# Optimization experiments

Measured on AMD Instinct MI355X. Metric: run time of the kernel, lower is better.

Reference implementation:

```python
import jax, jax.numpy as jnp
import numpy as np

N, E, D = 20000, 320000, 256
EPS = 1e-5


def setup_inputs() -> dict:
    key = jax.random.key(0)
    ks = jax.random.split(key, 12)
    s = 1.0 / np.sqrt(D)
    s2 = 1.0 / np.sqrt(2 * D)
    return {
        "node_embeddings": jax.random.normal(ks[0], (N, D), jnp.float32),
        "edge_index": jax.random.randint(ks[1], (2, E), 0, N, jnp.int64),
        "edge_embeddings": jax.random.normal(ks[2], (E, D), jnp.float32),
        # message MLP: Linear(D,D) -> GELU -> Linear(D,D)
        "W1m": jax.random.uniform(ks[3], (D, D), jnp.float32, -s, s),
        "b1m": jnp.zeros((D,), jnp.float32),
        "W2m": jax.random.uniform(ks[4], (D, D), jnp.float32, -s, s),
        "b2m": jnp.zeros((D,), jnp.float32),
        # update MLP: Linear(D,2D) -> GELU -> Linear(2D,D)
        "W1u": jax.random.uniform(ks[5], (D, 2 * D), jnp.float32, -s, s),
        "b1u": jnp.zeros((2 * D,), jnp.float32),
        "W2u": jax.random.uniform(ks[6], (2 * D, D), jnp.float32, -s2, s2),
        "b2u": jnp.zeros((D,), jnp.float32),
        # LayerNorm params
        "gamma": jnp.ones((D,), jnp.float32),
        "beta": jnp.zeros((D,), jnp.float32),
    }


def _layer_norm(x, gamma, beta):
    mu = jnp.mean(x, axis=-1, keepdims=True)
    var = jnp.mean(jnp.square(x - mu), axis=-1, keepdims=True)
    return (x - mu) * jax.lax.rsqrt(var + EPS) * gamma + beta


def reference(node_embeddings, edge_index, edge_embeddings,
              W1m, b1m, W2m, b2m, W1u, b1u, W2u, b2u, gamma, beta):
    src = edge_index[0]
    dst = edge_index[1]
    n = node_embeddings.shape[0]
    # gather + edge add + message MLP (exact erf GELU, as torch default)
    h = node_embeddings[src] + edge_embeddings           # [E, D]
    h = jax.nn.gelu(h @ W1m + b1m, approximate=False)
    messages = h @ W2m + b2m                             # [E, D]
    # scatter-mean aggregation
    agg = jax.ops.segment_sum(messages, dst, num_segments=n)  # [N, D]
    deg = jax.ops.segment_sum(jnp.ones((dst.shape[0], 1), node_embeddings.dtype),
                              dst, num_segments=n)            # [N, 1]
    agg = agg / jnp.maximum(deg, 1.0)
    # update MLP + residual + LayerNorm
    u = jax.nn.gelu(agg @ W1u + b1u, approximate=False) @ W2u + b2u
    return _layer_norm(node_embeddings + u, gamma, beta)
```

## Files before the change

kernel.cpp:

```cpp
#include <hip/hip_runtime.h>
#include <hip/hip_bf16.h>

#define N_NODES 20000
#define N_EDGES 320000

typedef __attribute__((ext_vector_type(8))) short short8;
typedef __attribute__((ext_vector_type(4))) float f32x4;

static __device__ __forceinline__ unsigned short f2bf(float f) {
  __hip_bfloat16 h = __float2bfloat16(f);
  union { __hip_bfloat16 h; unsigned short u; } cv; cv.h = h; return cv.u;
}

static __device__ __forceinline__ float bf2f(unsigned short u) {
  union { unsigned int u; float f; } cv; cv.u = ((unsigned int)u) << 16; return cv.f;
}

static __device__ __forceinline__ unsigned int pk2(float a, float b) {
  return (unsigned int)f2bf(a) | ((unsigned int)f2bf(b) << 16);
}

static __device__ __forceinline__ float gelu_f(float x) {
  float z = x * (2.3022082f + 0.1029432f * x * x);
  z = fminf(fmaxf(z, -30.0f), 30.0f);
  float t = exp2f(z);
  return x * t * __frcp_rn(1.0f + t);
}

#define SWZ(row, byteoff) ((byteoff) ^ (((row) & 7) << 4))
#define SWZU(b) ((b) ^ ((((b) >> 8) & 7) << 4))

__global__ void zero_kernel(float4* __restrict__ S4, int4* __restrict__ cnt4) {
  int idx = blockIdx.x * blockDim.x + threadIdx.x;
  S4[idx] = make_float4(0.f, 0.f, 0.f, 0.f);
  if (idx < N_NODES / 4) cnt4[idx] = make_int4(0, 0, 0, 0);
}

__global__ void pack_kernel(const float* __restrict__ W1m, const float* __restrict__ W2m,
                            const float* __restrict__ W1u, const float* __restrict__ W2u,
                            unsigned short* __restrict__ P1m, unsigned short* __restrict__ P2m,
                            unsigned short* __restrict__ P1u, unsigned short* __restrict__ P2u) {
  int idx = blockIdx.x * blockDim.x + threadIdx.x;
  const float* W; unsigned short* P; int K, Nc, local;
  if (idx < 65536)        { W = W1m; P = P1m; K = 256; Nc = 256; local = idx; }
  else if (idx < 131072)  { W = W2m; P = P2m; K = 256; Nc = 256; local = idx - 65536; }
  else if (idx < 262144)  { W = W1u; P = P1u; K = 256; Nc = 512; local = idx - 131072; }
  else                    { W = W2u; P = P2u; K = 512; Nc = 256; local = idx - 262144; }
  int frag = local >> 9, wi = local & 511;
  int l = wi >> 3, i = wi & 7;
  int kf = K >> 5;
  int cf = frag / kf, t = frag % kf;
  int k = t * 32 + (l >> 4) * 8 + i;
  int n = cf * 16 + (l & 15);
  P[local] = f2bf(W[(size_t)k * Nc + n]);
}

__global__ void hist_kernel(const int* __restrict__ dst, int* __restrict__ cnt) {
  int e = blockIdx.x * blockDim.x + threadIdx.x;
  atomicAdd(&cnt[dst[e]], 1);
}

__global__ __launch_bounds__(1024) void scan_kernel(const int* __restrict__ cnt,
                                                    int* __restrict__ rptr,
                                                    int* __restrict__ cur) {
  __shared__ int sums[1024];
  const int t = threadIdx.x;
  const int base = t * 20;
  int local[20];
  int s = 0;
#pragma unroll
  for (int i = 0; i < 20; ++i) {
    int idx = base + i;
    int v = (idx < N_NODES) ? cnt[idx] : 0;
    local[i] = s;
    s += v;
  }
  int v = s;
  sums[t] = v;
  for (int off = 1; off < 1024; off <<= 1) {
    __syncthreads();
    int o = (t >= off) ? sums[t - off] : 0;
    __syncthreads();
    v += o;
    sums[t] = v;
  }
  int excl = v - s;
#pragma unroll
  for (int i = 0; i < 20; ++i) {
    int idx = base + i;
    if (idx < N_NODES) { int p = excl + local[i]; rptr[idx] = p; cur[idx] = p; }
  }
  if (t == 1023) rptr[N_NODES] = v;
}

__global__ void scatter_kernel(const int* __restrict__ dst, int* __restrict__ cur,
                               int* __restrict__ perm) {
  int e = blockIdx.x * blockDim.x + threadIdx.x;
  int d = dst[e];
  int pos = atomicAdd(&cur[d], 1);
  perm[pos] = e;
}

__global__ __launch_bounds__(256) void edge_kernel(
    const float* __restrict__ node, const float* __restrict__ eemb,
    const int* __restrict__ src, const int* __restrict__ dst,
    const int* __restrict__ perm,
    const unsigned short* __restrict__ P1m, const float* __restrict__ b1m,
    float* __restrict__ S) {
  __shared__ unsigned short tA[64 * 256];
  __shared__ int dstS[64];
  const int tid = threadIdx.x;
  const int e0 = blockIdx.x * 64;
  {
    const int r = tid >> 2;
    const int cs = (tid & 3) * 64;
    const int e = perm[e0 + r];
    const int se = src[e];
    if ((tid & 3) == 0) dstS[r] = dst[e];
    const float* ep = eemb + (size_t)e * 256 + cs;
    const float* np = node + (size_t)se * 256 + cs;
#pragma unroll
    for (int i = 0; i < 8; ++i) {
      float4 a = *(const float4*)(ep + i * 8);
      float4 b = *(const float4*)(np + i * 8);
      float4 c = *(const float4*)(ep + i * 8 + 4);
      float4 d = *(const float4*)(np + i * 8 + 4);
      uint4 p;
      p.x = pk2(a.x + b.x, a.y + b.y);
      p.y = pk2(a.z + b.z, a.w + b.w);
      p.z = pk2(c.x + d.x, c.y + d.y);
      p.w = pk2(c.z + d.z, c.w + d.w);
      *(uint4*)((char*)tA + SWZ(r, r * 512 + (cs + i * 8) * 2)) = p;
    }
  }
  __syncthreads();

  const int w = tid >> 6, l = tid & 63;
  const int lr = l & 15, lh = l >> 4;
  f32x4 acc[4][4];
#pragma unroll
  for (int c = 0; c < 4; ++c) {
    float bb = b1m[w * 64 + c * 16 + lr];
#pragma unroll
    for (int r4 = 0; r4 < 4; ++r4) acc[r4][c] = f32x4{bb, bb, bb, bb};
  }
#pragma unroll
  for (int t = 0; t < 8; ++t) {
    short8 af[4], bfr[4];
#pragma unroll
    for (int r4 = 0; r4 < 4; ++r4) {
      int row = r4 * 16 + lr;
      af[r4] = *(const short8*)((const char*)tA + SWZ(row, row * 512 + t * 64 + lh * 16));
    }
#pragma unroll
    for (int c = 0; c < 4; ++c)
      bfr[c] = *(const short8*)(P1m + (size_t)(((w * 4 + c) * 8 + t) * 512 + l * 8));
#pragma unroll
    for (int r4 = 0; r4 < 4; ++r4)
#pragma unroll
      for (int c = 0; c < 4; ++c)
        acc[r4][c] = __builtin_amdgcn_mfma_f32_16x16x32_bf16(af[r4], bfr[c], acc[r4][c], 0, 0, 0);
  }
  __syncthreads();

#pragma unroll
  for (int r4 = 0; r4 < 4; ++r4)
#pragma unroll
    for (int c = 0; c < 4; ++c) {
      int col = w * 64 + c * 16 + lr;
#pragma unroll
      for (int j = 0; j < 4; ++j) {
        int row = r4 * 16 + lh * 4 + j;
        *(unsigned short*)((char*)tA + SWZ(row, row * 512 + col * 2)) =
            f2bf(gelu_f(acc[r4][c][j]));
      }
    }
  __syncthreads();

  {
    const int col = tid;
    const int r0 = 0, r1 = 32;
    float runA = 0.f, runB = 0.f;
    int curA = dstS[r0], curB = dstS[r1];
#pragma unroll 8
    for (int i = 0; i < 32; ++i) {
      int dA = dstS[r0 + i];
      int dB = dstS[r1 + i];
      float vA = bf2f(*(const unsigned short*)((const char*)tA +
                      SWZ(r0 + i, (r0 + i) * 512 + col * 2)));
      float vB = bf2f(*(const unsigned short*)((const char*)tA +
                      SWZ(r1 + i, (r1 + i) * 512 + col * 2)));
      if (dA != curA) { atomicAdd(&S[(size_t)curA * 256 + col], runA); runA = 0.f; curA = dA; }
      if (dB != curB) { atomicAdd(&S[(size_t)curB * 256 + col], runB); runB = 0.f; curB = dB; }
      runA += vA;
      runB += vB;
    }
    atomicAdd(&S[(size_t)curA * 256 + col], runA);
    atomicAdd(&S[(size_t)curB * 256 + col], runB);
  }
}

__global__ __launch_bounds__(256) void node_kernel(
    const float* __restrict__ node, const float* __restrict__ S, const int* __restrict__ rptr,
    const unsigned short* __restrict__ P2m, const float* __restrict__ b2m,
    const unsigned short* __restrict__ P1u, const float* __restrict__ b1u,
    const unsigned short* __restrict__ P2u, const float* __restrict__ b2u,
    const float* __restrict__ gamma, const float* __restrict__ beta,
    float* __restrict__ out) {
  __shared__ unsigned short tAB[2][64 * 256];
  __shared__ unsigned short tH[64 * 512];
  __shared__ float fmu[64], frs[64], fflag[64];
  float* tU = (float*)tAB;
  const int tid = threadIdx.x;
  const int n0 = blockIdx.x * 64;
  const int r = tid >> 2;
  const int cs = (tid & 3) * 64;
  const int n = n0 + r;
  const bool valid = n < N_NODES;
  {
    int dgi = valid ? (rptr[n + 1] - rptr[n]) : 0;
    float dg = (float)dgi;
    float rec = 1.0f / fmaxf(dg, 1.0f);
    if ((tid & 3) == 0) fflag[r] = (dgi > 0) ? 1.0f : 0.0f;
    const float4* sp = (const float4*)(S + (size_t)n * 256 + cs);
#pragma unroll
    for (int i = 0; i < 8; ++i) {
      float4 a = valid ? sp[2 * i]     : make_float4(0.f, 0.f, 0.f, 0.f);
      float4 b = valid ? sp[2 * i + 1] : make_float4(0.f, 0.f, 0.f, 0.f);
      uint4 p;
      p.x = pk2(a.x * rec, a.y * rec);
      p.y = pk2(a.z * rec, a.w * rec);
      p.z = pk2(b.x * rec, b.y * rec);
      p.w = pk2(b.z * rec, b.w * rec);
      *(uint4*)((char*)tAB[0] + SWZ(r, r * 512 + (cs + i * 8) * 2)) = p;
    }
  }
  __syncthreads();
  const int w = tid >> 6, l = tid & 63, lr = l & 15, lh = l >> 4;

  {
    f32x4 acc[4][4];
#pragma unroll
    for (int r4 = 0; r4 < 4; ++r4)
#pragma unroll
      for (int c = 0; c < 4; ++c) acc[r4][c] = f32x4{0.f, 0.f, 0.f, 0.f};
#pragma unroll
    for (int t = 0; t < 8; ++t) {
      short8 af[4], bfr[4];
#pragma unroll
      for (int r4 = 0; r4 < 4; ++r4) {
        int row = r4 * 16 + lr;
        af[r4] = *(const short8*)((const char*)tAB[0] + SWZ(row, row * 512 + t * 64 + lh * 16));
      }
#pragma unroll
      for (int c = 0; c < 4; ++c)
        bfr[c] = *(const short8*)(P2m + (size_t)(((w * 4 + c) * 8 + t) * 512 + l * 8));
#pragma unroll
      for (int r4 = 0; r4 < 4; ++r4)
#pragma unroll
        for (int c = 0; c < 4; ++c)
          acc[r4][c] = __builtin_amdgcn_mfma_f32_16x16x32_bf16(af[r4], bfr[c], acc[r4][c], 0, 0, 0);
    }
#pragma unroll
    for (int r4 = 0; r4 < 4; ++r4)
#pragma unroll
      for (int c = 0; c < 4; ++c) {
        int col = w * 64 + c * 16 + lr;
        float bm = b2m[col];
#pragma unroll
        for (int j = 0; j < 4; ++j) {
          int row = r4 * 16 + lh * 4 + j;
          float v = acc[r4][c][j] + fflag[row] * bm;
          *(unsigned short*)((char*)tAB[1] + SWZ(row, row * 512 + col * 2)) = f2bf(v);
        }
      }
  }
  __syncthreads();

  {
    f32x4 acc[4][8];
#pragma unroll
    for (int r4 = 0; r4 < 4; ++r4)
#pragma unroll
      for (int c = 0; c < 8; ++c) acc[r4][c] = f32x4{0.f, 0.f, 0.f, 0.f};
#pragma unroll
    for (int t = 0; t < 8; ++t) {
      short8 af[4], bfr[8];
#pragma unroll
      for (int r4 = 0; r4 < 4; ++r4) {
        int row = r4 * 16 + lr;
        af[r4] = *(const short8*)((const char*)tAB[1] + SWZ(row, row * 512 + t * 64 + lh * 16));
      }
#pragma unroll
      for (int c = 0; c < 8; ++c)
        bfr[c] = *(const short8*)(P1u + (size_t)(((w * 8 + c) * 8 + t) * 512 + l * 8));
#pragma unroll
      for (int r4 = 0; r4 < 4; ++r4)
#pragma unroll
        for (int c = 0; c < 8; ++c)
          acc[r4][c] = __builtin_amdgcn_mfma_f32_16x16x32_bf16(af[r4], bfr[c], acc[r4][c], 0, 0, 0);
    }
#pragma unroll
    for (int r4 = 0; r4 < 4; ++r4)
#pragma unroll
      for (int c = 0; c < 8; ++c) {
        int col = w * 128 + c * 16 + lr;
        float b1 = b1u[col];
#pragma unroll
        for (int j = 0; j < 4; ++j) {
          int row = r4 * 16 + lh * 4 + j;
          float v = gelu_f(acc[r4][c][j] + b1);
          *(unsigned short*)((char*)tH + SWZ(row, row * 1024 + col * 2)) = f2bf(v);
        }
      }
  }
  __syncthreads();

  {
    f32x4 acc[4][4];
#pragma unroll
    for (int r4 = 0; r4 < 4; ++r4)
#pragma unroll
      for (int c = 0; c < 4; ++c) acc[r4][c] = f32x4{0.f, 0.f, 0.f, 0.f};
#pragma unroll
    for (int t = 0; t < 16; ++t) {
      short8 af[4], bfr[4];
#pragma unroll
      for (int r4 = 0; r4 < 4; ++r4) {
        int row = r4 * 16 + lr;
        af[r4] = *(const short8*)((const char*)tH + SWZ(row, row * 1024 + t * 64 + lh * 16));
      }
#pragma unroll
      for (int c = 0; c < 4; ++c)
        bfr[c] = *(const short8*)(P2u + (size_t)(((w * 4 + c) * 16 + t) * 512 + l * 8));
#pragma unroll
      for (int r4 = 0; r4 < 4; ++r4)
#pragma unroll
        for (int c = 0; c < 4; ++c)
          acc[r4][c] = __builtin_amdgcn_mfma_f32_16x16x32_bf16(af[r4], bfr[c], acc[r4][c], 0, 0, 0);
    }
#pragma unroll
    for (int r4 = 0; r4 < 4; ++r4)
#pragma unroll
      for (int c = 0; c < 4; ++c) {
        int col = w * 64 + c * 16 + lr;
        float b2 = b2u[col];
#pragma unroll
        for (int j = 0; j < 4; ++j) {
          int row = r4 * 16 + lh * 4 + j;
          *(float*)((char*)tU + SWZU(row * 1024 + col * 4)) = acc[r4][c][j] + b2;
        }
      }
  }
  __syncthreads();

  {
    float sum = 0.f, sq = 0.f;
#pragma unroll
    for (int i = 0; i < 16; ++i) {
      int byte = SWZU(r * 1024 + (cs + i * 4) * 4);
      float4 v = *(float4*)((char*)tU + byte);
      if (valid) {
        const float4 nb = *(const float4*)(node + (size_t)n * 256 + cs + i * 4);
        v.x += nb.x; v.y += nb.y; v.z += nb.z; v.w += nb.w;
        *(float4*)((char*)tU + byte) = v;
      }
      sum += v.x + v.y + v.z + v.w;
      sq += v.x * v.x + v.y * v.y + v.z * v.z + v.w * v.w;
    }
    sum += __shfl_xor(sum, 1); sum += __shfl_xor(sum, 2);
    sq  += __shfl_xor(sq, 1);  sq  += __shfl_xor(sq, 2);
    if ((tid & 3) == 0) {
      float mu = sum * (1.0f / 256.0f);
      fmu[r] = mu;
      frs[r] = rsqrtf(fmaxf(sq * (1.0f / 256.0f) - mu * mu, 0.0f) + 1e-5f);
    }
  }
  __syncthreads();
#pragma unroll
  for (int i = 0; i < 16; ++i) {
    int f4 = i * 256 + tid;
    int row = f4 >> 6;
    int c4 = f4 & 63;
    int nn = n0 + row;
    if (nn < N_NODES) {
      float4 v = *(float4*)((char*)tU + SWZU(row * 1024 + c4 * 16));
      float mu = fmu[row], rs = frs[row];
      float4 g  = *(const float4*)(gamma + c4 * 4);
      float4 bt = *(const float4*)(beta + c4 * 4);
      float4 o;
      o.x = (v.x - mu) * rs * g.x + bt.x;
      o.y = (v.y - mu) * rs * g.y + bt.y;
      o.z = (v.z - mu) * rs * g.z + bt.z;
      o.w = (v.w - mu) * rs * g.w + bt.w;
      *(float4*)(out + (size_t)nn * 256 + c4 * 4) = o;
    }
  }
}

extern "C" void kernel_launch(void* const* d_in, const int* in_sizes, int n_in,
                              void* d_out, int out_size, void* d_ws, size_t ws_size,
                              hipStream_t stream) {
  const float* node = (const float*)d_in[0];
  const int* eidx = (const int*)d_in[1];
  const float* eemb = (const float*)d_in[2];
  const float* W1m = (const float*)d_in[3];
  const float* b1m = (const float*)d_in[4];
  const float* W2m = (const float*)d_in[5];
  const float* b2m = (const float*)d_in[6];
  const float* W1u = (const float*)d_in[7];
  const float* b1u = (const float*)d_in[8];
  const float* W2u = (const float*)d_in[9];
  const float* b2u = (const float*)d_in[10];
  const float* gamma = (const float*)d_in[11];
  const float* beta = (const float*)d_in[12];
  float* out = (float*)d_out;

  char* ws = (char*)d_ws;
  int* cnt  = (int*)ws;
  int* rptr = (int*)(ws + 81920);
  int* cur  = (int*)(ws + 163840);
  int* perm = (int*)(ws + 245760);
  unsigned short* P1m = (unsigned short*)(ws + 1525760);
  unsigned short* P2m = (unsigned short*)(ws + 1656832);
  unsigned short* P1u = (unsigned short*)(ws + 1787904);
  unsigned short* P2u = (unsigned short*)(ws + 2050048);
  const int* src = eidx;
  const int* dst = eidx + N_EDGES;

  zero_kernel<<<N_NODES * 64 / 256, 256, 0, stream>>>((float4*)out, (int4*)cnt);
  pack_kernel<<<393216 / 256, 256, 0, stream>>>(W1m, W2m, W1u, W2u, P1m, P2m, P1u, P2u);
  hist_kernel<<<N_EDGES / 256, 256, 0, stream>>>(dst, cnt);
  scan_kernel<<<1, 1024, 0, stream>>>(cnt, rptr, cur);
  scatter_kernel<<<N_EDGES / 256, 256, 0, stream>>>(dst, cur, perm);
  edge_kernel<<<N_EDGES / 64, 256, 0, stream>>>(node, eemb, src, dst, perm, P1m, b1m, out);
  node_kernel<<<(N_NODES + 63) / 64, 256, 0, stream>>>(node, out, rptr, P2m, b2m,
                                                       P1u, b1u, P2u, b2u, gamma, beta, out);
}
```

Measured before the change: 341.0 us.

## Halve edge/node tiles, reduce segments in registers, chunk update MLP hidden

Edge and node kernels now process 32 rows per block instead of 64, with launch bounds raised to allow more resident blocks. The edge kernel no longer writes GELU outputs back to LDS for a column-serial scan. Instead it finds destination segments with a wave ballot, reduces each segment through cross-lane shuffles, and issues atomics straight from registers. The node kernel splits the 512-wide update hidden layer into two 256-wide halves, accumulating into the second GEMM to shrink LDS and register use. The cost is more blocks, redundant weight fetches per row, and a per-segment loop that becomes serial when segments are short.

```diff
diff --git a/kernel.cpp b/kernel.cpp
--- a/kernel.cpp
+++ b/kernel.cpp
@@ -3,6 +3,8 @@
 
 #define N_NODES 20000
 #define N_EDGES 320000
+#define EBLK 32
+#define NBLK 32
 
 typedef __attribute__((ext_vector_type(8))) short short8;
 typedef __attribute__((ext_vector_type(4))) float f32x4;
@@ -10,10 +12,6 @@
 static __device__ __forceinline__ unsigned short f2bf(float f) {
   __hip_bfloat16 h = __float2bfloat16(f);
   union { __hip_bfloat16 h; unsigned short u; } cv; cv.h = h; return cv.u;
-}
-
-static __device__ __forceinline__ float bf2f(unsigned short u) {
-  union { unsigned int u; float f; } cv; cv.u = ((unsigned int)u) << 16; return cv.f;
 }
 
 static __device__ __forceinline__ unsigned int pk2(float a, float b) {
@@ -101,26 +99,26 @@
   perm[pos] = e;
 }
 
-__global__ __launch_bounds__(256) void edge_kernel(
+__global__ __launch_bounds__(256, 8) void edge_kernel(
     const float* __restrict__ node, const float* __restrict__ eemb,
     const int* __restrict__ src, const int* __restrict__ dst,
     const int* __restrict__ perm,
     const unsigned short* __restrict__ P1m, const float* __restrict__ b1m,
     float* __restrict__ S) {
-  __shared__ unsigned short tA[64 * 256];
-  __shared__ int dstS[64];
+  __shared__ unsigned short tA[EBLK * 256];
+  __shared__ int dstS[EBLK];
   const int tid = threadIdx.x;
-  const int e0 = blockIdx.x * 64;
+  const int e0 = blockIdx.x * EBLK;
   {
-    const int r = tid >> 2;
-    const int cs = (tid & 3) * 64;
+    const int r = tid >> 3;
+    const int cs = (tid & 7) * 32;
     const int e = perm[e0 + r];
     const int se = src[e];
-    if ((tid & 3) == 0) dstS[r] = dst[e];
+    if ((tid & 7) == 0) dstS[r] = dst[e];
     const float* ep = eemb + (size_t)e * 256 + cs;
     const float* np = node + (size_t)se * 256 + cs;
 #pragma unroll
-    for (int i = 0; i < 8; ++i) {
+    for (int i = 0; i < 4; ++i) {
       float4 a = *(const float4*)(ep + i * 8);
       float4 b = *(const float4*)(np + i * 8);
       float4 c = *(const float4*)(ep + i * 8 + 4);
@@ -137,96 +135,102 @@
 
   const int w = tid >> 6, l = tid & 63;
   const int lr = l & 15, lh = l >> 4;
-  f32x4 acc[4][4];
+  f32x4 acc[2][4];
 #pragma unroll
   for (int c = 0; c < 4; ++c) {
     float bb = b1m[w * 64 + c * 16 + lr];
-#pragma unroll
-    for (int r4 = 0; r4 < 4; ++r4) acc[r4][c] = f32x4{bb, bb, bb, bb};
-  }
-#pragma unroll
-  for (int t = 0; t < 8; ++t) {
-    short8 af[4], bfr[4];
-#pragma unroll
-    for (int r4 = 0; r4 < 4; ++r4) {
-      int row = r4 * 16 + lr;
-      af[r4] = *(const short8*)((const char*)tA + SWZ(row, row * 512 + t * 64 + lh * 16));
-    }
+    acc[0][c] = f32x4{bb, bb, bb, bb};
+    acc[1][c] = f32x4{bb, bb, bb, bb};
+  }
+#pragma unroll
+  for (int kt = 0; kt < 8; ++kt) {
+    const int row0 = lr, row1 = 16 + lr;
+    short8 af0 = *(const short8*)((const char*)tA + SWZ(row0, row0 * 512 + kt * 64 + lh * 16));
+    short8 af1 = *(const short8*)((const char*)tA + SWZ(row1, row1 * 512 + kt * 64 + lh * 16));
+#pragma unroll
+    for (int c = 0; c < 4; ++c) {
+      short8 bfr = *(const short8*)(P1m + (size_t)(((w * 4 + c) * 8 + kt) * 512 + l * 8));
+      acc[0][c] = __builtin_amdgcn_mfma_f32_16x16x32_bf16(af0, bfr, acc[0][c], 0, 0, 0);
+      acc[1][c] = __builtin_amdgcn_mfma_f32_16x16x32_bf16(af1, bfr, acc[1][c], 0, 0, 0);
+    }
+  }
+
+#pragma unroll
+  for (int r4 = 0; r4 < 2; ++r4)
 #pragma unroll
     for (int c = 0; c < 4; ++c)
-      bfr[c] = *(const short8*)(P1m + (size_t)(((w * 4 + c) * 8 + t) * 512 + l * 8));
-#pragma unroll
-    for (int r4 = 0; r4 < 4; ++r4)
-#pragma unroll
-      for (int c = 0; c < 4; ++c)
-        acc[r4][c] = __builtin_amdgcn_mfma_f32_16x16x32_bf16(af[r4], bfr[c], acc[r4][c], 0, 0, 0);
-  }
-  __syncthreads();
-
-#pragma unroll
-  for (int r4 = 0; r4 < 4; ++r4)
-#pragma unroll
-    for (int c = 0; c < 4; ++c) {
-      int col = w * 64 + c * 16 + lr;
+#pragma unroll
+      for (int j = 0; j < 4; ++j)
+        acc[r4][c][j] = gelu_f(acc[r4][c][j]);
+
+  const int dv = dstS[l & 31];
+  const int pv = __shfl(dv, (l - 1) & 63);
+  const bool bflag = (l < 32) && ((l == 0) || (dv != pv));
+  const unsigned long long mask = __ballot(bflag);
+  const int nseg = __popcll(mask);
+  int sid[2][4];
+#pragma unroll
+  for (int r4 = 0; r4 < 2; ++r4)
+#pragma unroll
+    for (int j = 0; j < 4; ++j) {
+      int row = r4 * 16 + lh * 4 + j;
+      sid[r4][j] = __popcll(mask & ((2ULL << row) - 1)) - 1;
+    }
+  unsigned long long rem = mask;
+  for (int s = 0; s < nseg; ++s) {
+    const int rowf = __builtin_ctzll(rem);
+    rem &= rem - 1;
+    const int dseg = __shfl(dv, rowf);
+    float p0 = 0.f, p1 = 0.f, p2 = 0.f, p3 = 0.f;
+#pragma unroll
+    for (int r4 = 0; r4 < 2; ++r4)
 #pragma unroll
       for (int j = 0; j < 4; ++j) {
-        int row = r4 * 16 + lh * 4 + j;
-        *(unsigned short*)((char*)tA + SWZ(row, row * 512 + col * 2)) =
-            f2bf(gelu_f(acc[r4][c][j]));
-      }
-    }
-  __syncthreads();
-
-  {
-    const int col = tid;
-    const int r0 = 0, r1 = 32;
-    float runA = 0.f, runB = 0.f;
-    int curA = dstS[r0], curB = dstS[r1];
-#pragma unroll 8
-    for (int i = 0; i < 32; ++i) {
-      int dA = dstS[r0 + i];
-      int dB = dstS[r1 + i];
-      float vA = bf2f(*(const unsigned short*)((const char*)tA +
-                      SWZ(r0 + i, (r0 + i) * 512 + col * 2)));
-      float vB = bf2f(*(const unsigned short*)((const char*)tA +
-                      SWZ(r1 + i, (r1 + i) * 512 + col * 2)));
-      if (dA != curA) { atomicAdd(&S[(size_t)curA * 256 + col], runA); runA = 0.f; curA = dA; }
-      if (dB != curB) { atomicAdd(&S[(size_t)curB * 256 + col], runB); runB = 0.f; curB = dB; }
-      runA += vA;
-      runB += vB;
-    }
-    atomicAdd(&S[(size_t)curA * 256 + col], runA);
-    atomicAdd(&S[(size_t)curB * 256 + col], runB);
-  }
-}
-
-__global__ __launch_bounds__(256) void node_kernel(
+        bool m = (sid[r4][j] == s);
+        p0 += m ? acc[r4][0][j] : 0.f;
+        p1 += m ? acc[r4][1][j] : 0.f;
+        p2 += m ? acc[r4][2][j] : 0.f;
+        p3 += m ? acc[r4][3][j] : 0.f;
+      }
+    p0 += __shfl_xor(p0, 16); p0 += __shfl_xor(p0, 32);
+    p1 += __shfl_xor(p1, 16); p1 += __shfl_xor(p1, 32);
+    p2 += __shfl_xor(p2, 16); p2 += __shfl_xor(p2, 32);
+    p3 += __shfl_xor(p3, 16); p3 += __shfl_xor(p3, 32);
+    if (lh == 0) {
+      float* Sp = S + (size_t)dseg * 256 + w * 64 + lr;
+      atomicAdd(Sp, p0);
+      atomicAdd(Sp + 16, p1);
+      atomicAdd(Sp + 32, p2);
+      atomicAdd(Sp + 48, p3);
+    }
+  }
+}
+
+__global__ __launch_bounds__(256, 4) void node_kernel(
     const float* __restrict__ node, const float* __restrict__ S, const int* __restrict__ rptr,
     const unsigned short* __restrict__ P2m, const float* __restrict__ b2m,
     const unsigned short* __restrict__ P1u, const float* __restrict__ b1u,
     const unsigned short* __restrict__ P2u, const float* __restrict__ b2u,
     const float* __restrict__ gamma, const float* __restrict__ beta,
     float* __restrict__ out) {
-  __shared__ unsigned short tAB[2][64 * 256];
-  __shared__ unsigned short tH[64 * 512];
-  __shared__ float fmu[64], frs[64], fflag[64];
+  __shared__ unsigned short tAB[2][NBLK * 256];
+  __shared__ unsigned short tH[NBLK * 256];
+  __shared__ float fmu[NBLK], frs[NBLK], fflag[NBLK];
   float* tU = (float*)tAB;
   const int tid = threadIdx.x;
-  const int n0 = blockIdx.x * 64;
-  const int r = tid >> 2;
-  const int cs = (tid & 3) * 64;
+  const int n0 = blockIdx.x * NBLK;
+  const int r = tid >> 3;
+  const int cs = (tid & 7) * 32;
   const int n = n0 + r;
-  const bool valid = n < N_NODES;
   {
-    int dgi = valid ? (rptr[n + 1] - rptr[n]) : 0;
-    float dg = (float)dgi;
-    float rec = 1.0f / fmaxf(dg, 1.0f);
-    if ((tid & 3) == 0) fflag[r] = (dgi > 0) ? 1.0f : 0.0f;
-    const float4* sp = (const float4*)(S + (size_t)n * 256 + cs);
-#pragma unroll
-    for (int i = 0; i < 8; ++i) {
-      float4 a = valid ? sp[2 * i]     : make_float4(0.f, 0.f, 0.f, 0.f);
-      float4 b = valid ? sp[2 * i + 1] : make_float4(0.f, 0.f, 0.f, 0.f);
+    int dgi = rptr[n + 1] - rptr[n];
+    float rec = 1.0f / fmaxf((float)dgi, 1.0f);
+    if ((tid & 7) == 0) fflag[r] = (dgi > 0) ? 1.0f : 0.0f;
+    const float* sp = S + (size_t)n * 256 + cs;
+#pragma unroll
+    for (int i = 0; i < 4; ++i) {
+      float4 a = *(const float4*)(sp + i * 8);
+      float4 b = *(const float4*)(sp + i * 8 + 4);
       uint4 p;
       p.x = pk2(a.x * rec, a.y * rec);
       p.y = pk2(a.z * rec, a.w * rec);
@@ -239,30 +243,25 @@
   const int w = tid >> 6, l = tid & 63, lr = l & 15, lh = l >> 4;
 
   {
-    f32x4 acc[4][4];
-#pragma unroll
-    for (int r4 = 0; r4 < 4; ++r4)
+    f32x4 acc[2][4];
+#pragma unroll
+    for (int r4 = 0; r4 < 2; ++r4)
 #pragma unroll
       for (int c = 0; c < 4; ++c) acc[r4][c] = f32x4{0.f, 0.f, 0.f, 0.f};
 #pragma unroll
     for (int t = 0; t < 8; ++t) {
-      short8 af[4], bfr[4];
-#pragma unroll
-      for (int r4 = 0; r4 < 4; ++r4) {
-        int row = r4 * 16 + lr;
-        af[r4] = *(const short8*)((const char*)tAB[0] + SWZ(row, row * 512 + t * 64 + lh * 16));
-      }
-#pragma unroll
-      for (int c = 0; c < 4; ++c)
-        bfr[c] = *(const short8*)(P2m + (size_t)(((w * 4 + c) * 8 + t) * 512 + l * 8));
-#pragma unroll
-      for (int r4 = 0; r4 < 4; ++r4)
-#pragma unroll
-        for (int c = 0; c < 4; ++c)
-          acc[r4][c] = __builtin_amdgcn_mfma_f32_16x16x32_bf16(af[r4], bfr[c], acc[r4][c], 0, 0, 0);
-    }
-#pragma unroll
-    for (int r4 = 0; r4 < 4; ++r4)
+      const int row0 = lr, row1 = 16 + lr;
+      short8 af0 = *(const short8*)((const char*)tAB[0] + SWZ(row0, row0 * 512 + t * 64 + lh * 16));
+      short8 af1 = *(const short8*)((const char*)tAB[0] + SWZ(row1, row1 * 512 + t * 64 + lh * 16));
+#pragma unroll
+      for (int c = 0; c < 4; ++c) {
+        short8 bfr = *(const short8*)(P2m + (size_t)(((w * 4 + c) * 8 + t) * 512 + l * 8));
+        acc[0][c] = __builtin_amdgcn_mfma_f32_16x16x32_bf16(af0, bfr, acc[0][c], 0, 0, 0);
+        acc[1][c] = __builtin_amdgcn_mfma_f32_16x16x32_bf16(af1, bfr, acc[1][c], 0, 0, 0);
+      }
+    }
+#pragma unroll
+    for (int r4 = 0; r4 < 2; ++r4)
 #pragma unroll
       for (int c = 0; c < 4; ++c) {
         int col = w * 64 + c * 16 + lr;
@@ -277,100 +276,93 @@
   }
   __syncthreads();
 
-  {
-    f32x4 acc[4][8];
-#pragma unroll
-    for (int r4 = 0; r4 < 4; ++r4)
-#pragma unroll
-      for (int c = 0; c < 8; ++c) acc[r4][c] = f32x4{0.f, 0.f, 0.f, 0.f};
-#pragma unroll
-    for (int t = 0; t < 8; ++t) {
-      short8 af[4], bfr[8];
-#pragma unroll
-      for (int r4 = 0; r4 < 4; ++r4) {
-        int row = r4 * 16 + lr;
-        af[r4] = *(const short8*)((const char*)tAB[1] + SWZ(row, row * 512 + t * 64 + lh * 16));
-      }
-#pragma unroll
-      for (int c = 0; c < 8; ++c)
-        bfr[c] = *(const short8*)(P1u + (size_t)(((w * 8 + c) * 8 + t) * 512 + l * 8));
-#pragma unroll
-      for (int r4 = 0; r4 < 4; ++r4)
-#pragma unroll
-        for (int c = 0; c < 8; ++c)
-          acc[r4][c] = __builtin_amdgcn_mfma_f32_16x16x32_bf16(af[r4], bfr[c], acc[r4][c], 0, 0, 0);
-    }
-#pragma unroll
-    for (int r4 = 0; r4 < 4; ++r4)
-#pragma unroll
-      for (int c = 0; c < 8; ++c) {
-        int col = w * 128 + c * 16 + lr;
-        float b1 = b1u[col];
-#pragma unroll
-        for (int j = 0; j < 4; ++j) {
-          int row = r4 * 16 + lh * 4 + j;
-          float v = gelu_f(acc[r4][c][j] + b1);
-          *(unsigned short*)((char*)tH + SWZ(row, row * 1024 + col * 2)) = f2bf(v);
+  f32x4 acc3[2][4];
+#pragma unroll
+  for (int c = 0; c < 4; ++c) {
+    float bb = b2u[w * 64 + c * 16 + lr];
+    acc3[0][c] = f32x4{bb, bb, bb, bb};
+    acc3[1][c] = f32x4{bb, bb, bb, bb};
+  }
+#pragma unroll
+  for (int half = 0; half < 2; ++half) {
+    {
+      f32x4 acc[2][4];
+#pragma unroll
+      for (int r4 = 0; r4 < 2; ++r4)
+#pragma unroll
+        for (int c = 0; c < 4; ++c) acc[r4][c] = f32x4{0.f, 0.f, 0.f, 0.f};
+#pragma unroll
+      for (int t = 0; t < 8; ++t) {
+        const int row0 = lr, row1 = 16 + lr;
+        short8 af0 = *(const short8*)((const char*)tAB[1] + SWZ(row0, row0 * 512 + t * 64 + lh * 16));
+        short8 af1 = *(const short8*)((const char*)tAB[1] + SWZ(row1, row1 * 512 + t * 64 + lh * 16));
+#pragma unroll
+        for (int c = 0; c < 4; ++c) {
+          short8 bfr = *(const short8*)(P1u + (size_t)(((half * 16 + w * 4 + c) * 8 + t) * 512 + l * 8));
+          acc[0][c] = __builtin_amdgcn_mfma_f32_16x16x32_bf16(af0, bfr, acc[0][c], 0, 0, 0);
+          acc[1][c] = __builtin_amdgcn_mfma_f32_16x16x32_bf16(af1, bfr, acc[1][c], 0, 0, 0);
         }
       }
-  }
-  __syncthreads();
-
-  {
-    f32x4 acc[4][4];
-#pragma unroll
-    for (int r4 = 0; r4 < 4; ++r4)
-#pragma unroll
-      for (int c = 0; c < 4; ++c) acc[r4][c] = f32x4{0.f, 0.f, 0.f, 0.f};
-#pragma unroll
-    for (int t = 0; t < 16; ++t) {
-      short8 af[4], bfr[4];
-#pragma unroll
-      for (int r4 = 0; r4 < 4; ++r4) {
-        int row = r4 * 16 + lr;
-        af[r4] = *(const short8*)((const char*)tH + SWZ(row, row * 1024 + t * 64 + lh * 16));
-      }
-#pragma unroll
-      for (int c = 0; c < 4; ++c)
-        bfr[c] = *(const short8*)(P2u + (size_t)(((w * 4 + c) * 16 + t) * 512 + l * 8));
-#pragma unroll
-      for (int r4 = 0; r4 < 4; ++r4)
-#pragma unroll
-        for (int c = 0; c < 4; ++c)
-          acc[r4][c] = __builtin_amdgcn_mfma_f32_16x16x32_bf16(af[r4], bfr[c], acc[r4][c], 0, 0, 0);
-    }
-#pragma unroll
-    for (int r4 = 0; r4 < 4; ++r4)
-#pragma unroll
-      for (int c = 0; c < 4; ++c) {
-        int col = w * 64 + c * 16 + lr;
-        float b2 = b2u[col];
-#pragma unroll
-        for (int j = 0; j < 4; ++j) {
-          int row = r4 * 16 + lh * 4 + j;
-          *(float*)((char*)tU + SWZU(row * 1024 + col * 4)) = acc[r4][c][j] + b2;
+#pragma unroll
+      for (int r4 = 0; r4 < 2; ++r4)
+#pragma unroll
+        for (int c = 0; c < 4; ++c) {
+          int col = w * 64 + c * 16 + lr;
+          float b1 = b1u[half * 256 + col];
+#pragma unroll
+          for (int j = 0; j < 4; ++j) {
+            int row = r4 * 16 + lh * 4 + j;
+            float v = gelu_f(acc[r4][c][j] + b1);
+            *(unsigned short*)((char*)tH + SWZ(row, row * 512 + col * 2)) = f2bf(v);
+          }
         }
-      }
-  }
+    }
+    __syncthreads();
+    {
+#pragma unroll
+      for (int tt = 0; tt < 8; ++tt) {
+        const int row0 = lr, row1 = 16 + lr;
+        short8 af0 = *(const short8*)((const char*)tH + SWZ(row0, row0 * 512 + tt * 64 + lh * 16));
+        short8 af1 = *(const short8*)((const char*)tH + SWZ(row1, row1 * 512 + tt * 64 + lh * 16));
+#pragma unroll
+        for (int c = 0; c < 4; ++c) {
+          short8 bfr = *(const short8*)(P2u + (size_t)(((w * 4 + c) * 16 + half * 8 + tt) * 512 + l * 8));
+          acc3[0][c] = __builtin_amdgcn_mfma_f32_16x16x32_bf16(af0, bfr, acc3[0][c], 0, 0, 0);
+          acc3[1][c] = __builtin_amdgcn_mfma_f32_16x16x32_bf16(af1, bfr, acc3[1][c], 0, 0, 0);
+        }
+      }
+    }
+    __syncthreads();
+  }
+
+#pragma unroll
+  for (int r4 = 0; r4 < 2; ++r4)
+#pragma unroll
+    for (int c = 0; c < 4; ++c) {
+      int col = w * 64 + c * 16 + lr;
+#pragma unroll
+      for (int j = 0; j < 4; ++j) {
+        int row = r4 * 16 + lh * 4 + j;
+        *(float*)((char*)tU + SWZU(row * 1024 + col * 4)) = acc3[r4][c][j];
+      }
+    }
   __syncthreads();
 
   {
     float sum = 0.f, sq = 0.f;
 #pragma unroll
-    for (int i = 0; i < 16; ++i) {
+    for (int i = 0; i < 8; ++i) {
       int byte = SWZU(r * 1024 + (cs + i * 4) * 4);
       float4 v = *(float4*)((char*)tU + byte);
-      if (valid) {
-        const float4 nb = *(const float4*)(node + (size_t)n * 256 + cs + i * 4);
-        v.x += nb.x; v.y += nb.y; v.z += nb.z; v.w += nb.w;
-        *(float4*)((char*)tU + byte) = v;
-      }
+      const float4 nb = *(const float4*)(node + (size_t)n * 256 + cs + i * 4);
+      v.x += nb.x; v.y += nb.y; v.z += nb.z; v.w += nb.w;
+      *(float4*)((char*)tU + byte) = v;
       sum += v.x + v.y + v.z + v.w;
       sq += v.x * v.x + v.y * v.y + v.z * v.z + v.w * v.w;
     }
-    sum += __shfl_xor(sum, 1); sum += __shfl_xor(sum, 2);
-    sq  += __shfl_xor(sq, 1);  sq  += __shfl_xor(sq, 2);
-    if ((tid & 3) == 0) {
+    sum += __shfl_xor(sum, 1); sum += __shfl_xor(sum, 2); sum += __shfl_xor(sum, 4);
+    sq  += __shfl_xor(sq, 1);  sq  += __shfl_xor(sq, 2);  sq  += __shfl_xor(sq, 4);
+    if ((tid & 7) == 0) {
       float mu = sum * (1.0f / 256.0f);
       fmu[r] = mu;
       frs[r] = rsqrtf(fmaxf(sq * (1.0f / 256.0f) - mu * mu, 0.0f) + 1e-5f);
@@ -378,23 +370,20 @@
   }
   __syncthreads();
 #pragma unroll
-  for (int i = 0; i < 16; ++i) {
+  for (int i = 0; i < 8; ++i) {
     int f4 = i * 256 + tid;
     int row = f4 >> 6;
     int c4 = f4 & 63;
-    int nn = n0 + row;
-    if (nn < N_NODES) {
-      float4 v = *(float4*)((char*)tU + SWZU(row * 1024 + c4 * 16));
-      float mu = fmu[row], rs = frs[row];
-      float4 g  = *(const float4*)(gamma + c4 * 4);
-      float4 bt = *(const float4*)(beta + c4 * 4);
-      float4 o;
-      o.x = (v.x - mu) * rs * g.x + bt.x;
-      o.y = (v.y - mu) * rs * g.y + bt.y;
-      o.z = (v.z - mu) * rs * g.z + bt.z;
-      o.w = (v.w - mu) * rs * g.w + bt.w;
-      *(float4*)(out + (size_t)nn * 256 + c4 * 4) = o;
-    }
+    float4 v = *(float4*)((char*)tU + SWZU(row * 1024 + c4 * 16));
+    float mu = fmu[row], rs = frs[row];
+    float4 g  = *(const float4*)(gamma + c4 * 4);
+    float4 bt = *(const float4*)(beta + c4 * 4);
+    float4 o;
+    o.x = (v.x - mu) * rs * g.x + bt.x;
+    o.y = (v.y - mu) * rs * g.y + bt.y;
+    o.z = (v.z - mu) * rs * g.z + bt.z;
+    o.w = (v.w - mu) * rs * g.w + bt.w;
+    *(float4*)(out + (size_t)(n0 + row) * 256 + c4 * 4) = o;
   }
 }
 
@@ -433,7 +422,7 @@
   hist_kernel<<<N_EDGES / 256, 256, 0, stream>>>(dst, cnt);
   scan_kernel<<<1, 1024, 0, stream>>>(cnt, rptr, cur);
   scatter_kernel<<<N_EDGES / 256, 256, 0, stream>>>(dst, cur, perm);
-  edge_kernel<<<N_EDGES / 64, 256, 0, stream>>>(node, eemb, src, dst, perm, P1m, b1m, out);
-  node_kernel<<<(N_NODES + 63) / 64, 256, 0, stream>>>(node, out, rptr, P2m, b2m,
-                                                       P1u, b1u, P2u, b2u, gamma, beta, out);
-}
+  edge_kernel<<<N_EDGES / EBLK, 256, 0, stream>>>(node, eemb, src, dst, perm, P1m, b1m, out);
+  node_kernel<<<N_NODES / NBLK, 256, 0, stream>>>(node, out, rptr, P2m, b2m,
+                                                  P1u, b1u, P2u, b2u, gamma, beta, out);
+}
```

Result: slower. 374.5 us (+9.8%).
